# Kernel tuning notes

Hardware: AMD Instinct MI355X
Metric: run time of the kernel (lower is better)

## Reference

```python
import jax, jax.numpy as jnp
import numpy as np

EMBED = 1024
HEADS = 16
HEAD_DIM = EMBED // HEADS


def setup_inputs() -> dict:
    key = jax.random.key(0)
    ks = jax.random.split(key, 11)
    B, S, D = 2, 2048, EMBED
    scale = 1.0 / np.sqrt(D)
    inp = {
        "q": jax.random.normal(ks[0], (B, S, D), jnp.float32),
        "k": jax.random.normal(ks[1], (B, S, D), jnp.float32),
        "v": jax.random.normal(ks[2], (B, S, D), jnp.float32),
        "Wq": jax.random.normal(ks[3], (D, D), jnp.float32) * scale,
        "bq": jnp.zeros((D,), jnp.float32),
        "Wk": jax.random.normal(ks[4], (D, D), jnp.float32) * scale,
        "bk": jnp.zeros((D,), jnp.float32),
        "Wv": jax.random.normal(ks[5], (D, D), jnp.float32) * scale,
        "bv": jnp.zeros((D,), jnp.float32),
        "Wo": jax.random.normal(ks[6], (D, D), jnp.float32) * scale,
        "bo": jnp.zeros((D,), jnp.float32),
    }
    return inp


def _split_heads(x):
    b, n, c = x.shape
    return x.reshape(b, n, HEADS, c // HEADS).transpose(0, 2, 1, 3)  # [b,h,n,dh]


def reference(q, k, v, Wq, bq, Wk, bk, Wv, bv, Wo, bo):
    qh = _split_heads(q @ Wq + bq)
    kh = _split_heads(k @ Wk + bk)
    vh = _split_heads(v @ Wv + bv)
    scale = 1.0 / jnp.sqrt(jnp.asarray(HEAD_DIM, qh.dtype))
    att = jnp.einsum("bhqd,bhkd->bhqk", qh, kh) * scale
    att = jax.nn.softmax(att, axis=-1)
    out = jnp.einsum("bhqk,bhkd->bhqd", att, vh)
    b, h, n, dh = out.shape
    out = out.transpose(0, 2, 1, 3).reshape(b, n, h * dh)
    return out @ Wo + bo
```

## Files before the change

### kernel.cpp

```cpp
#include <hip/hip_runtime.h>
#include <hip/hip_bf16.h>
#include <stdint.h>

typedef unsigned short u16;
typedef __bf16 bf16x8 __attribute__((ext_vector_type(8)));
typedef float f32x4 __attribute__((ext_vector_type(4)));
typedef unsigned int u32x4 __attribute__((ext_vector_type(4)));
typedef unsigned int u32x2 __attribute__((ext_vector_type(2)));

#define S_LEN 2048
#define DMODEL 1024
#define NHEAD 16
#define DHEAD 64
#define MROWS 4096

__device__ __forceinline__ u16 f2b(float f) {
  __hip_bfloat16 h = __float2bfloat16(f);
  union { __hip_bfloat16 h; u16 u; } c;
  c.h = h;
  return c.u;
}
__device__ __forceinline__ unsigned int pk2(float lo, float hi) {
  return (unsigned int)f2b(lo) | ((unsigned int)f2b(hi) << 16);
}

__device__ __forceinline__ void gload16(const void* g, void* l) {
  __builtin_amdgcn_global_load_lds(
      (const __attribute__((address_space(1))) unsigned int*)(uintptr_t)g,
      (__attribute__((address_space(3))) unsigned int*)(uintptr_t)l,
      16, 0, 0);
}

__global__ __launch_bounds__(256) void prep(
    const float* __restrict__ q, const float* __restrict__ k, const float* __restrict__ v,
    const float* __restrict__ Wq, const float* __restrict__ Wk,
    const float* __restrict__ Wv, const float* __restrict__ Wo,
    u16* __restrict__ Qx, u16* __restrict__ Kx, u16* __restrict__ Vx,
    u16* __restrict__ Wqt, u16* __restrict__ Wkt,
    u16* __restrict__ Wvt, u16* __restrict__ Wot) {
  __shared__ u16 tile[64][65];
  const int z = blockIdx.z;
  const int tid = threadIdx.x;
  if (z < 3) {
    const float* src = (z == 0) ? q : (z == 1) ? k : v;
    u16* dst = (z == 0) ? Qx : (z == 1) ? Kx : Vx;
    const size_t i8 = ((size_t)blockIdx.x * 256 + tid) * 8;
    float4 a = *(const float4*)(src + i8);
    float4 b = *(const float4*)(src + i8 + 4);
    u16 o[8];
    o[0] = f2b(a.x); o[1] = f2b(a.y); o[2] = f2b(a.z); o[3] = f2b(a.w);
    o[4] = f2b(b.x); o[5] = f2b(b.y); o[6] = f2b(b.z); o[7] = f2b(b.w);
    *(u32x4*)(dst + i8) = *(const u32x4*)o;
    return;
  }
  if (blockIdx.x >= 256) return;
  const int zz = z - 3;
  const float* W = (zz == 0) ? Wq : (zz == 1) ? Wk : (zz == 2) ? Wv : Wo;
  u16* Wt = (zz == 0) ? Wqt : (zz == 1) ? Wkt : (zz == 2) ? Wvt : Wot;
  const int n0 = (blockIdx.x & 15) * 64, k0 = (blockIdx.x >> 4) * 64;
#pragma unroll
  for (int j = 0; j < 16; j++) {
    int idx = j * 256 + tid;
    int r = idx >> 6, c = idx & 63;
    tile[r][c] = f2b(W[(size_t)(k0 + r) * DMODEL + n0 + c]);
  }
  __syncthreads();
#pragma unroll
  for (int j = 0; j < 16; j++) {
    int idx = j * 256 + tid;
    int r = idx >> 6, c = idx & 63;
    Wt[(size_t)(n0 + r) * DMODEL + k0 + c] = tile[c][r];
  }
}

template <int MODE>
__device__ __forceinline__ void gemm_body(const u16* __restrict__ A,
                                          const u16* __restrict__ Bt,
                                          const float* __restrict__ bias,
                                          void* __restrict__ Cv) {
  constexpr int K = DMODEL;
  __shared__ u16 As[128 * 32];
  __shared__ u16 Bs[128 * 32];
  const int tid = threadIdx.x;
  const int wave = tid >> 6, lane = tid & 63;
  const int quad = lane >> 4, l15 = lane & 15;
  const int wr = wave >> 1, wc = wave & 1;
  const int brow = blockIdx.y, bcol = blockIdx.x;

  f32x4 acc[4][4] = {};

  for (int k0 = 0; k0 < K; k0 += 32) {
    __syncthreads();
#pragma unroll
    for (int t = 0; t < 2; t++) {
      const int slot = t * 256 + wave * 64 + lane;
      const int row = slot >> 2;
      const int col = (slot & 3) << 3;
      const int ldsb = (t * 256 + wave * 64) * 8;
      gload16(A + (size_t)(brow * 128 + row) * K + k0 + col, As + ldsb);
      gload16(Bt + (size_t)(bcol * 128 + row) * K + k0 + col, Bs + ldsb);
    }
    __syncthreads();

    bf16x8 af[4], bfm[4];
#pragma unroll
    for (int i = 0; i < 4; i++)
      af[i] = *(const bf16x8*)(As + (wr * 64 + i * 16 + l15) * 32 + quad * 8);
#pragma unroll
    for (int j = 0; j < 4; j++)
      bfm[j] = *(const bf16x8*)(Bs + (wc * 64 + j * 16 + l15) * 32 + quad * 8);
#pragma unroll
    for (int i = 0; i < 4; i++)
#pragma unroll
      for (int j = 0; j < 4; j++)
        acc[i][j] = __builtin_amdgcn_mfma_f32_16x16x32_bf16(af[i], bfm[j], acc[i][j], 0, 0, 0);
  }

#pragma unroll
  for (int i = 0; i < 4; i++)
#pragma unroll
    for (int j = 0; j < 4; j++) {
      const int col = bcol * 128 + wc * 64 + j * 16 + l15;
      const float bv = bias[col];
      if (MODE == 2) {
        const int srow = brow * 128 + wr * 64 + i * 16 + quad * 4;
        const int bb = srow >> 11, s = srow & (S_LEN - 1);
        u32x2 pd;
        pd.x = pk2(acc[i][j][0] + bv, acc[i][j][1] + bv);
        pd.y = pk2(acc[i][j][2] + bv, acc[i][j][3] + bv);
        *(u32x2*)((u16*)Cv + ((size_t)(bb * 1024 + col)) * S_LEN + s) = pd;
      } else {
#pragma unroll
        for (int r = 0; r < 4; r++) {
          const int row = brow * 128 + wr * 64 + i * 16 + quad * 4 + r;
          if (MODE == 1)
            ((float*)Cv)[(size_t)row * DMODEL + col] = acc[i][j][r] + bv;
          else
            ((u16*)Cv)[(size_t)row * DMODEL + col] = f2b(acc[i][j][r] + bv);
        }
      }
    }
}

__global__ __launch_bounds__(256) void gemm_qkv(
    const u16* __restrict__ Qx, const u16* __restrict__ Kx, const u16* __restrict__ Vx,
    const u16* __restrict__ Wqt, const u16* __restrict__ Wkt, const u16* __restrict__ Wvt,
    const float* __restrict__ bq, const float* __restrict__ bk, const float* __restrict__ bv,
    u16* __restrict__ Qp, u16* __restrict__ Kp, u16* __restrict__ Vt) {
  const int z = blockIdx.z;
  if (z == 2) {
    gemm_body<2>(Vx, Wvt, bv, Vt);
  } else {
    const u16* A = (z == 0) ? Qx : Kx;
    const u16* Bt = (z == 0) ? Wqt : Wkt;
    const float* bias = (z == 0) ? bq : bk;
    u16* C = (z == 0) ? Qp : Kp;
    gemm_body<0>(A, Bt, bias, C);
  }
}

__global__ __launch_bounds__(256) void gemm_out(
    const u16* __restrict__ A, const u16* __restrict__ Bt,
    const float* __restrict__ bias, float* __restrict__ C) {
  gemm_body<1>(A, Bt, bias, C);
}

#define EXP2SCALE 0.180336880112f
__global__ __launch_bounds__(256) void attn(const u16* __restrict__ Qp,
                                            const u16* __restrict__ Kp,
                                            const u16* __restrict__ Vt,
                                            u16* __restrict__ Op) {
  __shared__ u16 Ks[64 * 64];
  __shared__ u16 Vs[64 * 64];
  __shared__ u16 Ps[64 * 64];

  const int tid = threadIdx.x;
  const int wave = tid >> 6, lane = tid & 63;
  const int quad = lane >> 4, l15 = lane & 15;
  const int b = blockIdx.z, h = blockIdx.y, s0 = blockIdx.x * 64;

  const size_t baseK = ((size_t)(b * S_LEN)) * DMODEL + h * DHEAD;
  const size_t baseV = ((size_t)((b * NHEAD + h) * DHEAD)) * S_LEN;

  bf16x8 b1;
  {
    union { u16 a[8]; bf16x8 v; } c;
    u16 one = (l15 == 0) ? 0x3F80 : 0;
#pragma unroll
    for (int j = 0; j < 8; j++) c.a[j] = one;
    b1 = c.v;
  }

  bf16x8 qf[2];
#pragma unroll
  for (int kx = 0; kx < 2; kx++)
    qf[kx] = *(const bf16x8*)(Qp +
        ((size_t)(b * S_LEN + s0 + wave * 16 + l15)) * DMODEL +
        h * DHEAD + kx * 32 + quad * 8);

  f32x4 oacc[4] = {};
  f32x4 lacc = {};

  u32x4 kreg[2], vreg[2];
#pragma unroll
  for (int t = 0; t < 2; t++) {
    int idx = t * 256 + tid;
    int r = idx >> 3, c = (idx & 7) * 8;
    kreg[t] = *(const u32x4*)(Kp + baseK + (size_t)r * DMODEL + c);
    vreg[t] = *(const u32x4*)(Vt + baseV + (size_t)r * S_LEN + c);
  }

  for (int kt = 0; kt < 32; kt++) {
    __syncthreads();
#pragma unroll
    for (int t = 0; t < 2; t++) {
      int idx = t * 256 + tid;
      int r = idx >> 3, c = (idx & 7) * 8;
      int di = (r * 64 + c) ^ ((r & 7) << 3);
      *(u32x4*)(Ks + di) = kreg[t];
      *(u32x4*)(Vs + di) = vreg[t];
    }
    __syncthreads();

    if (kt < 31) {
#pragma unroll
      for (int t = 0; t < 2; t++) {
        int idx = t * 256 + tid;
        int r = idx >> 3, c = (idx & 7) * 8;
        kreg[t] = *(const u32x4*)(Kp + baseK + (size_t)((kt + 1) * 64 + r) * DMODEL + c);
        vreg[t] = *(const u32x4*)(Vt + baseV + (size_t)r * S_LEN + (kt + 1) * 64 + c);
      }
    }

    f32x4 sfT[4] = {};
    __builtin_amdgcn_s_setprio(1);
#pragma unroll
    for (int n = 0; n < 4; n++) {
#pragma unroll
      for (int kx = 0; kx < 2; kx++) {
        bf16x8 ka = *(const bf16x8*)(Ks +
            ((((n * 16 + l15) * 64) + kx * 32 + quad * 8) ^ ((l15 & 7) << 3)));
        sfT[n] = __builtin_amdgcn_mfma_f32_16x16x32_bf16(ka, qf[kx], sfT[n], 0, 0, 0);
      }
    }
    __builtin_amdgcn_s_setprio(0);

#pragma unroll
    for (int n = 0; n < 4; n++) {
      float p0 = __builtin_amdgcn_exp2f(sfT[n][0] * EXP2SCALE);
      float p1 = __builtin_amdgcn_exp2f(sfT[n][1] * EXP2SCALE);
      float p2 = __builtin_amdgcn_exp2f(sfT[n][2] * EXP2SCALE);
      float p3 = __builtin_amdgcn_exp2f(sfT[n][3] * EXP2SCALE);
      u32x2 pd;
      pd.x = pk2(p0, p1);
      pd.y = pk2(p2, p3);
      int row = wave * 16 + l15;
      *(u32x2*)(Ps + ((row * 64 + n * 16 + quad * 4) ^ ((row & 7) << 3))) = pd;
    }

    __builtin_amdgcn_s_setprio(1);
#pragma unroll
    for (int kx = 0; kx < 2; kx++) {
      int prow = wave * 16 + l15;
      bf16x8 ap = *(const bf16x8*)(Ps +
          ((prow * 64 + kx * 32 + quad * 8) ^ ((prow & 7) << 3)));
      lacc = __builtin_amdgcn_mfma_f32_16x16x32_bf16(ap, b1, lacc, 0, 0, 0);
#pragma unroll
      for (int n = 0; n < 4; n++) {
        bf16x8 bv = *(const bf16x8*)(Vs +
            ((((n * 16 + l15) * 64) + kx * 32 + quad * 8) ^ ((l15 & 7) << 3)));
        oacc[n] = __builtin_amdgcn_mfma_f32_16x16x32_bf16(ap, bv, oacc[n], 0, 0, 0);
      }
    }
    __builtin_amdgcn_s_setprio(0);
  }

  float inv[4];
#pragma unroll
  for (int r = 0; r < 4; r++)
    inv[r] = 1.0f / __shfl(lacc[r], quad * 16);
#pragma unroll
  for (int n = 0; n < 4; n++)
#pragma unroll
    for (int r = 0; r < 4; r++) {
      int row = s0 + wave * 16 + quad * 4 + r;
      int col = h * DHEAD + n * 16 + l15;
      Op[((size_t)(b * S_LEN + row)) * DMODEL + col] = f2b(oacc[n][r] * inv[r]);
    }
}

extern "C" void kernel_launch(void* const* d_in, const int* in_sizes, int n_in,
                              void* d_out, int out_size, void* d_ws, size_t ws_size,
                              hipStream_t stream) {
  const float* q  = (const float*)d_in[0];
  const float* k  = (const float*)d_in[1];
  const float* v  = (const float*)d_in[2];
  const float* Wq = (const float*)d_in[3];
  const float* bq = (const float*)d_in[4];
  const float* Wk = (const float*)d_in[5];
  const float* bk = (const float*)d_in[6];
  const float* Wv = (const float*)d_in[7];
  const float* bv = (const float*)d_in[8];
  const float* Wo = (const float*)d_in[9];
  const float* bo = (const float*)d_in[10];

  char* w = (char*)d_ws;
  const size_t WSZ = (size_t)DMODEL * DMODEL * 2;
  const size_t XSZ = (size_t)MROWS * DMODEL * 2;
  u16* Wqt = (u16*)(w);
  u16* Wkt = (u16*)(w + WSZ);
  u16* Wvt = (u16*)(w + 2 * WSZ);
  u16* Wot = (u16*)(w + 3 * WSZ);
  u16* Qx  = (u16*)(w + 4 * WSZ);
  u16* Kx  = (u16*)(w + 4 * WSZ + XSZ);
  u16* Vx  = (u16*)(w + 4 * WSZ + 2 * XSZ);
  u16* Qp  = (u16*)(w + 4 * WSZ + 3 * XSZ);
  u16* Kp  = (u16*)(w + 4 * WSZ + 4 * XSZ);
  u16* Vt  = (u16*)(w + 4 * WSZ + 5 * XSZ);
  u16* Op  = (u16*)(w + 4 * WSZ + 6 * XSZ);

  prep<<<dim3(2048, 1, 7), 256, 0, stream>>>(q, k, v, Wq, Wk, Wv, Wo,
                                             Qx, Kx, Vx, Wqt, Wkt, Wvt, Wot);
  gemm_qkv<<<dim3(8, 32, 3), 256, 0, stream>>>(Qx, Kx, Vx, Wqt, Wkt, Wvt,
                                               bq, bk, bv, Qp, Kp, Vt);
  attn<<<dim3(32, 16, 2), 256, 0, stream>>>(Qp, Kp, Vt, Op);
  gemm_out<<<dim3(8, 32, 1), 256, 0, stream>>>(Op, Wot, bo, (float*)d_out);
}
```

Measured before the change: 241.1 us.

## Double-buffer attention K/V tiles with direct global-to-LDS loads and swizzle GEMM blocks

The attention kernel now keeps two LDS buffers for K and V and fills them with asynchronous global-to-LDS loads (gload16), issuing the next tile before computing the current one. This drops the register staging and the per-tile LDS store pass. The XOR swizzle is folded into the source column addresses. The GEMM blocks are also remapped so that adjacent launched blocks cover different row tiles, to change L2 reuse. The change costs extra LDS, and the barrier placement relies on the async loads having completed before each __syncthreads.

```diff
diff --git a/kernel.cpp b/kernel.cpp
--- a/kernel.cpp
+++ b/kernel.cpp
@@ -85,7 +85,9 @@
   const int wave = tid >> 6, lane = tid & 63;
   const int quad = lane >> 4, l15 = lane & 15;
   const int wr = wave >> 1, wc = wave & 1;
-  const int brow = blockIdx.y, bcol = blockIdx.x;
+  const int lid = blockIdx.y * 8 + blockIdx.x;
+  const int sw = (lid & 7) * 32 + (lid >> 3);
+  const int bcol = sw & 7, brow = sw >> 3;
 
   f32x4 acc[4][4] = {};
 
@@ -166,12 +168,61 @@
 }
 
 #define EXP2SCALE 0.180336880112f
+
+#define ISSUE_KV(ksb, vsb)              \
+  do {                                  \
+    gload16(pK0, (ksb) + dstu);         \
+    gload16(pK1, (ksb) + 2048 + dstu);  \
+    gload16(pV0, (vsb) + dstu);         \
+    gload16(pV1, (vsb) + 2048 + dstu);  \
+    pK0 += 64 * DMODEL; pK1 += 64 * DMODEL; \
+    pV0 += 64; pV1 += 64;               \
+  } while (0)
+
+#define TILE_COMPUTE(ksb, vsb)                                                   \
+  do {                                                                           \
+    f32x4 sfT[4] = {};                                                           \
+    __builtin_amdgcn_s_setprio(1);                                               \
+    _Pragma("unroll") for (int n = 0; n < 4; n++) {                              \
+      _Pragma("unroll") for (int kx = 0; kx < 2; kx++) {                         \
+        bf16x8 ka = *(const bf16x8*)((ksb) +                                     \
+            ((((n * 16 + l15) * 64) + kx * 32 + quad * 8) ^ ((l15 & 7) << 3)));  \
+        sfT[n] = __builtin_amdgcn_mfma_f32_16x16x32_bf16(ka, qf[kx], sfT[n], 0, 0, 0); \
+      }                                                                          \
+    }                                                                            \
+    __builtin_amdgcn_s_setprio(0);                                               \
+    _Pragma("unroll") for (int n = 0; n < 4; n++) {                              \
+      float p0 = __builtin_amdgcn_exp2f(sfT[n][0] * EXP2SCALE);                  \
+      float p1 = __builtin_amdgcn_exp2f(sfT[n][1] * EXP2SCALE);                  \
+      float p2 = __builtin_amdgcn_exp2f(sfT[n][2] * EXP2SCALE);                  \
+      float p3 = __builtin_amdgcn_exp2f(sfT[n][3] * EXP2SCALE);                  \
+      u32x2 pd;                                                                  \
+      pd.x = pk2(p0, p1);                                                        \
+      pd.y = pk2(p2, p3);                                                        \
+      int prow = wave * 16 + l15;                                                \
+      *(u32x2*)(Ps + ((prow * 64 + n * 16 + quad * 4) ^ ((prow & 7) << 3))) = pd;\
+    }                                                                            \
+    __builtin_amdgcn_s_setprio(1);                                               \
+    _Pragma("unroll") for (int kx = 0; kx < 2; kx++) {                           \
+      int prow = wave * 16 + l15;                                                \
+      bf16x8 ap = *(const bf16x8*)(Ps +                                          \
+          ((prow * 64 + kx * 32 + quad * 8) ^ ((prow & 7) << 3)));               \
+      lacc = __builtin_amdgcn_mfma_f32_16x16x32_bf16(ap, b1, lacc, 0, 0, 0);     \
+      _Pragma("unroll") for (int n = 0; n < 4; n++) {                            \
+        bf16x8 bv = *(const bf16x8*)((vsb) +                                     \
+            ((((n * 16 + l15) * 64) + kx * 32 + quad * 8) ^ ((l15 & 7) << 3)));  \
+        oacc[n] = __builtin_amdgcn_mfma_f32_16x16x32_bf16(ap, bv, oacc[n], 0, 0, 0); \
+      }                                                                          \
+    }                                                                            \
+    __builtin_amdgcn_s_setprio(0);                                               \
+  } while (0)
+
 __global__ __launch_bounds__(256) void attn(const u16* __restrict__ Qp,
                                             const u16* __restrict__ Kp,
                                             const u16* __restrict__ Vt,
                                             u16* __restrict__ Op) {
-  __shared__ u16 Ks[64 * 64];
-  __shared__ u16 Vs[64 * 64];
+  __shared__ u16 Ks0[64 * 64], Ks1[64 * 64];
+  __shared__ u16 Vs0[64 * 64], Vs1[64 * 64];
   __shared__ u16 Ps[64 * 64];
 
   const int tid = threadIdx.x;
@@ -182,6 +233,14 @@
   const size_t baseK = ((size_t)(b * S_LEN)) * DMODEL + h * DHEAD;
   const size_t baseV = ((size_t)((b * NHEAD + h) * DHEAD)) * S_LEN;
 
+  const int r0 = tid >> 3;
+  const int cg = (tid & 7) ^ (r0 & 7);
+  const u16* pK0 = Kp + baseK + (size_t)r0 * DMODEL + cg * 8;
+  const u16* pK1 = pK0 + (size_t)32 * DMODEL;
+  const u16* pV0 = Vt + baseV + (size_t)r0 * S_LEN + cg * 8;
+  const u16* pV1 = pV0 + (size_t)32 * S_LEN;
+  const int dstu = wave * 512;
+
   bf16x8 b1;
   {
     union { u16 a[8]; bf16x8 v; } c;
@@ -201,78 +260,16 @@
   f32x4 oacc[4] = {};
   f32x4 lacc = {};
 
-  u32x4 kreg[2], vreg[2];
-#pragma unroll
-  for (int t = 0; t < 2; t++) {
-    int idx = t * 256 + tid;
-    int r = idx >> 3, c = (idx & 7) * 8;
-    kreg[t] = *(const u32x4*)(Kp + baseK + (size_t)r * DMODEL + c);
-    vreg[t] = *(const u32x4*)(Vt + baseV + (size_t)r * S_LEN + c);
-  }
-
-  for (int kt = 0; kt < 32; kt++) {
+  ISSUE_KV(Ks0, Vs0);
+
+#pragma unroll 1
+  for (int kt = 0; kt < 32; kt += 2) {
     __syncthreads();
-#pragma unroll
-    for (int t = 0; t < 2; t++) {
-      int idx = t * 256 + tid;
-      int r = idx >> 3, c = (idx & 7) * 8;
-      int di = (r * 64 + c) ^ ((r & 7) << 3);
-      *(u32x4*)(Ks + di) = kreg[t];
-      *(u32x4*)(Vs + di) = vreg[t];
-    }
+    ISSUE_KV(Ks1, Vs1);
+    TILE_COMPUTE(Ks0, Vs0);
     __syncthreads();
-
-    if (kt < 31) {
-#pragma unroll
-      for (int t = 0; t < 2; t++) {
-        int idx = t * 256 + tid;
-        int r = idx >> 3, c = (idx & 7) * 8;
-        kreg[t] = *(const u32x4*)(Kp + baseK + (size_t)((kt + 1) * 64 + r) * DMODEL + c);
-        vreg[t] = *(const u32x4*)(Vt + baseV + (size_t)r * S_LEN + (kt + 1) * 64 + c);
-      }
-    }
-
-    f32x4 sfT[4] = {};
-    __builtin_amdgcn_s_setprio(1);
-#pragma unroll
-    for (int n = 0; n < 4; n++) {
-#pragma unroll
-      for (int kx = 0; kx < 2; kx++) {
-        bf16x8 ka = *(const bf16x8*)(Ks +
-            ((((n * 16 + l15) * 64) + kx * 32 + quad * 8) ^ ((l15 & 7) << 3)));
-        sfT[n] = __builtin_amdgcn_mfma_f32_16x16x32_bf16(ka, qf[kx], sfT[n], 0, 0, 0);
-      }
-    }
-    __builtin_amdgcn_s_setprio(0);
-
-#pragma unroll
-    for (int n = 0; n < 4; n++) {
-      float p0 = __builtin_amdgcn_exp2f(sfT[n][0] * EXP2SCALE);
-      float p1 = __builtin_amdgcn_exp2f(sfT[n][1] * EXP2SCALE);
-      float p2 = __builtin_amdgcn_exp2f(sfT[n][2] * EXP2SCALE);
-      float p3 = __builtin_amdgcn_exp2f(sfT[n][3] * EXP2SCALE);
-      u32x2 pd;
-      pd.x = pk2(p0, p1);
-      pd.y = pk2(p2, p3);
-      int row = wave * 16 + l15;
-      *(u32x2*)(Ps + ((row * 64 + n * 16 + quad * 4) ^ ((row & 7) << 3))) = pd;
-    }
-
-    __builtin_amdgcn_s_setprio(1);
-#pragma unroll
-    for (int kx = 0; kx < 2; kx++) {
-      int prow = wave * 16 + l15;
-      bf16x8 ap = *(const bf16x8*)(Ps +
-          ((prow * 64 + kx * 32 + quad * 8) ^ ((prow & 7) << 3)));
-      lacc = __builtin_amdgcn_mfma_f32_16x16x32_bf16(ap, b1, lacc, 0, 0, 0);
-#pragma unroll
-      for (int n = 0; n < 4; n++) {
-        bf16x8 bv = *(const bf16x8*)(Vs +
-            ((((n * 16 + l15) * 64) + kx * 32 + quad * 8) ^ ((l15 & 7) << 3)));
-        oacc[n] = __builtin_amdgcn_mfma_f32_16x16x32_bf16(ap, bv, oacc[n], 0, 0, 0);
-      }
-    }
-    __builtin_amdgcn_s_setprio(0);
+    if (kt + 2 < 32) ISSUE_KV(Ks0, Vs0);
+    TILE_COMPUTE(Ks1, Vs1);
   }
 
   float inv[4];
```

After: 233.1 us. -3.3%, faster.
